# Performance work log

Hardware: AMD Instinct MI355X
Metric: run time of the kernel (lower is better)

## Reference

```python
import jax, jax.numpy as jnp
import numpy as np

DIM = 768
HEADS = 12
HEAD_DIM = DIM // HEADS
EPS_ATTN = 1e-6
LN_EPS = 1e-5


def _piece_weight():
    # BlockDistanceConv with num_patches_per_side=16, patch_group_size=16 -> 4x4 blocks
    bps = 4
    centers = np.array([[i + 0.5, j + 0.5] for i in range(bps) for j in range(bps)], dtype=np.float32)
    d = np.linalg.norm(centers[:, None, :] - centers[None, :, :], axis=-1)
    mat = np.cos(d / d.max() * np.pi / 4.0)  # 'cos' transform
    mat = mat / mat.sum(axis=0, keepdims=True)
    return jnp.asarray(mat, dtype=jnp.float32)  # [16, 16], out = W @ x over piece channels


def setup_inputs() -> dict:
    key = jax.random.key(0)
    ks = jax.random.split(key, 4)
    B, N, W, C = 128, 16, 16, DIM
    x = jax.random.normal(ks[0], (B, N, W, C), dtype=jnp.float32)
    ln_gamma = jnp.ones((C,), dtype=jnp.float32)
    ln_beta = jnp.zeros((C,), dtype=jnp.float32)
    w_qkv = jax.random.normal(ks[1], (C, 3 * C), dtype=jnp.float32) * (C ** -0.5)
    w_out = jax.random.normal(ks[2], (C, C), dtype=jnp.float32) * (C ** -0.5)
    b_out = jnp.zeros((C,), dtype=jnp.float32)
    w_piece = _piece_weight()
    return {"x": x, "ln_gamma": ln_gamma, "ln_beta": ln_beta, "w_qkv": w_qkv,
            "w_out": w_out, "b_out": b_out, "w_piece": w_piece}


def reference(x, ln_gamma, ln_beta, w_qkv, w_out, b_out, w_piece):
    B, N, W, C = x.shape
    H, D = HEADS, HEAD_DIM
    # LayerNorm over channel dim
    mu = jnp.mean(x, axis=-1, keepdims=True)
    var = jnp.mean((x - mu) ** 2, axis=-1, keepdims=True)
    xn = (x - mu) * jax.lax.rsqrt(var + LN_EPS) * ln_gamma + ln_beta
    # qkv projection (no bias)
    qkv = xn @ w_qkv  # [B,N,W,3C]
    q, k, v = jnp.split(qkv, 3, axis=-1)
    # relu kernel feature map
    q = jax.nn.relu(q) + EPS_ATTN
    k = jax.nn.relu(k) + EPS_ATTN
    # split heads: 'b n w (h d) -> b h n w d'
    def heads(t):
        return t.reshape(B, N, W, H, D).transpose(0, 3, 1, 2, 4)
    q, k, v = heads(q), heads(k), heads(v)
    # per-window kv = k^T v  (sum over window positions w)  -> [B,H,N,D,D]
    kv = jnp.einsum('bhnwd,bhnwe->bhnde', k, v)
    # BlockDistanceConv: 1x1 conv mixing over piece dim N with fixed weights
    kv = jnp.einsum('ij,bhjde->bhide', w_piece, kv)
    # out = q @ kv  -> [B,H,N,W,D]
    out = jnp.einsum('bhnwd,bhnde->bhnwe', q, kv)
    # merge heads: 'b h n w d -> b n w (h d)'
    out = out.transpose(0, 2, 3, 1, 4).reshape(B, N, W, H * D)
    # output projection (dropout is identity in eval)
    return out @ w_out + b_out
```

## Files before the change

kernel.cpp:

```cpp
#include <hip/hip_runtime.h>

#define DIM 768
#define HEADS 12
#define TOK 32768

typedef unsigned short ushort_t;
typedef __attribute__((ext_vector_type(8))) short short8v;
typedef __attribute__((ext_vector_type(4))) float f32x4;
typedef __attribute__((ext_vector_type(4))) unsigned short us4;

__device__ __forceinline__ ushort_t f2bf(float x) {
  union { float f; unsigned u; } c; c.f = x;
  unsigned r = (c.u + 0x7FFFu + ((c.u >> 16) & 1u)) >> 16;
  return (ushort_t)r;
}

__device__ __forceinline__ void gload_lds16(const void* g, void* l) {
  __builtin_amdgcn_global_load_lds((const __attribute__((address_space(1))) void*)g,
                                   (__attribute__((address_space(3))) void*)l, 16, 0, 0);
}

#define FENCE asm volatile("" ::: "memory")
#define SCHED0 __builtin_amdgcn_sched_barrier(0)
#define BARRIER do { FENCE; SCHED0; __builtin_amdgcn_s_barrier(); SCHED0; FENCE; } while (0)
#define LGK0 asm volatile("s_waitcnt lgkmcnt(0)" ::: "memory")
#define VM0  asm volatile("s_waitcnt vmcnt(0)" ::: "memory")
#define VM3  asm volatile("s_waitcnt vmcnt(3)" ::: "memory")

__global__ __launch_bounds__(256) void ln_kernel(const float* __restrict__ x,
                                                 const float* __restrict__ g,
                                                 const float* __restrict__ be,
                                                 ushort_t* __restrict__ xn) {
  int lane = threadIdx.x & 63;
  int row = blockIdx.x * 4 + (threadIdx.x >> 6);
  const float4* rx = (const float4*)(x + (size_t)row * DIM);
  float4 v[3];
  float s = 0.f, sq = 0.f;
  #pragma unroll
  for (int c = 0; c < 3; ++c) {
    v[c] = rx[lane + 64 * c];
    s  += v[c].x + v[c].y + v[c].z + v[c].w;
    sq += v[c].x * v[c].x + v[c].y * v[c].y + v[c].z * v[c].z + v[c].w * v[c].w;
  }
  #pragma unroll
  for (int off = 32; off; off >>= 1) {
    s  += __shfl_xor(s, off);
    sq += __shfl_xor(sq, off);
  }
  float mu  = s * (1.0f / DIM);
  float var = sq * (1.0f / DIM) - mu * mu;
  float rs  = rsqrtf(var + 1e-5f);
  us4* orow = (us4*)(xn + (size_t)row * DIM);
  const float4* gv = (const float4*)g;
  const float4* bv = (const float4*)be;
  #pragma unroll
  for (int c = 0; c < 3; ++c) {
    float4 gg = gv[lane + 64 * c];
    float4 bb = bv[lane + 64 * c];
    us4 pk;
    pk[0] = f2bf((v[c].x - mu) * rs * gg.x + bb.x);
    pk[1] = f2bf((v[c].y - mu) * rs * gg.y + bb.y);
    pk[2] = f2bf((v[c].z - mu) * rs * gg.z + bb.z);
    pk[3] = f2bf((v[c].w - mu) * rs * gg.w + bb.w);
    orow[lane + 64 * c] = pk;
  }
}

__global__ __launch_bounds__(256) void convT2(const float* __restrict__ s0,
                                              ushort_t* __restrict__ d0,
                                              const float* __restrict__ s1,
                                              ushort_t* __restrict__ d1) {
  int z = blockIdx.z;
  if (z && blockIdx.x >= DIM / 32) return;
  const float* src = z ? s1 : s0;
  ushort_t* dst = z ? d1 : d0;
  int Ccol = z ? DIM : 3 * DIM;
  const int R = DIM;
  __shared__ float tile[32][33];
  int c0 = blockIdx.x * 32, r0 = blockIdx.y * 32;
  int tx = threadIdx.x & 31, ty = threadIdx.x >> 5;
  #pragma unroll
  for (int i = 0; i < 32; i += 8)
    tile[ty + i][tx] = src[(size_t)(r0 + ty + i) * Ccol + c0 + tx];
  __syncthreads();
  #pragma unroll
  for (int i = 0; i < 32; i += 8)
    dst[(size_t)(c0 + ty + i) * R + r0 + tx] = f2bf(tile[tx][ty + i]);
}

__global__ __launch_bounds__(512, 2) void gemm_8ph(const ushort_t* __restrict__ A,
                                                   const ushort_t* __restrict__ Bt,
                                                   ushort_t* __restrict__ qbf,
                                                   ushort_t* __restrict__ kbf,
                                                   ushort_t* __restrict__ vTbf) {
  extern __shared__ __align__(16) char lds[];
  const int Kb = DIM * 2;
  const int N = 3 * DIM;
  const int nbn = N / 256;
  const size_t GHalf = (size_t)64 * Kb;

  int bid = blockIdx.x;
  int qd = gridDim.x >> 3;
  int wid = (bid & 7) * qd + (bid >> 3);
  int bm = wid / nbn, bn = wid % nbn;
  int row0 = bm * 256, col0 = bn * 256;
  int t = threadIdx.x;
  int lane = t & 63, wave = t >> 6;
  int wr = wave >> 2, wc = wave & 3;

  const char* Ag = (const char*)A + (size_t)row0 * Kb;
  const char* Bg = (const char*)Bt + (size_t)col0 * Kb;

  int o0 = t * 16;
  int sr = o0 >> 7;
  int skb = (o0 & 127) ^ ((sr & 7) << 4);
  size_t goff = (size_t)sr * Kb + skb;

  #define STG(Gbase, Lbase, kt)                                               \
    do {                                                                      \
      gload_lds16((Gbase) + goff + (size_t)(kt) * 128, lds + (Lbase) + o0);   \
      gload_lds16((Gbase) + goff + GHalf + (size_t)(kt) * 128,                \
                  lds + (Lbase) + o0 + 8192);                                 \
    } while (0)

  int fr = lane & 15, fkb = (lane >> 4) << 4;
  int swz = (fr & 7) << 4;
  int kb0 = fkb ^ swz;
  int kb1 = (64 + fkb) ^ swz;
  int laA = (wr * 128 + fr) * 128;
  int laB = 32768 + (wc * 64 + fr) * 128;

  #define LOAD_A(dst, dbase, mq)                                              \
    _Pragma("unroll") for (int mi = 0; mi < 4; ++mi) {                        \
      dst[mi][0] = *(const short8v*)(lds + (dbase) + laA + (mq)*8192 + mi*2048 + kb0); \
      dst[mi][1] = *(const short8v*)(lds + (dbase) + laA + (mq)*8192 + mi*2048 + kb1); \
    }
  #define LOAD_B(dst, dbase, nq)                                              \
    _Pragma("unroll") for (int ni = 0; ni < 2; ++ni) {                        \
      dst[ni][0] = *(const short8v*)(lds + (dbase) + laB + (nq)*4096 + ni*2048 + kb0); \
      dst[ni][1] = *(const short8v*)(lds + (dbase) + laB + (nq)*4096 + ni*2048 + kb1); \
    }
  #define MFMA16(av, bv, mq, nq)                                              \
    do {                                                                      \
      SCHED0;                                                                 \
      __builtin_amdgcn_s_setprio(1);                                          \
      _Pragma("unroll") for (int mi = 0; mi < 4; ++mi)                        \
        _Pragma("unroll") for (int ni = 0; ni < 2; ++ni) {                    \
          acc[(mq)*4+mi][(nq)*2+ni] = __builtin_amdgcn_mfma_f32_16x16x32_bf16(\
              av[mi][0], bv[ni][0], acc[(mq)*4+mi][(nq)*2+ni], 0, 0, 0);      \
          acc[(mq)*4+mi][(nq)*2+ni] = __builtin_amdgcn_mfma_f32_16x16x32_bf16(\
              av[mi][1], bv[ni][1], acc[(mq)*4+mi][(nq)*2+ni], 0, 0, 0);      \
        }                                                                     \
      __builtin_amdgcn_s_setprio(0);                                          \
    } while (0)

  STG(Ag, 0, 0);  STG(Ag + 128 * Kb, 16384, 0);
  STG(Bg, 32768, 0);  STG(Bg + 128 * Kb, 49152, 0);
  STG(Ag, 65536, 1);  STG(Ag + 128 * Kb, 65536 + 16384, 1);
  STG(Bg, 65536 + 32768, 1);
  asm volatile("s_waitcnt vmcnt(6)" ::: "memory");
  BARRIER;

  short8v aR0[4][2], aR1[4][2], bR0[2][2], bR1[2][2];
  LOAD_A(aR0, 0, 0); LOAD_B(bR0, 0, 0);

  f32x4 acc[8][4] = {};
  for (int it = 0; it < 6; ++it) {
    const int d0 = 0, d1 = 65536;
    int t1k = 2 * it + 1, t2k = 2 * it + 2, t3k = 2 * it + 3;
    bool st = (it < 5);
    LOAD_A(aR1, d0, 1);
    STG(Bg + 128 * Kb, d1 + 49152, t1k);
    MFMA16(aR0, bR0, 0, 0);
    BARRIER;
    LOAD_B(bR1, d0, 1);
    MFMA16(aR1, bR0, 1, 0);
    BARRIER;
    if (st) { STG(Ag, d0, t2k); STG(Ag + 128 * Kb, d0 + 16384, t2k); }
    MFMA16(aR0, bR1, 0, 1);
    if (st) asm volatile("s_waitcnt vmcnt(4)" ::: "memory");
    else    asm volatile("s_waitcnt vmcnt(0)" ::: "memory");
    BARRIER;
    LOAD_A(aR0, d1, 0); LOAD_B(bR0, d1, 0);
    if (st) STG(Bg, d0 + 32768, t2k);
    MFMA16(aR1, bR1, 1, 1);
    BARRIER;
    LOAD_A(aR1, d1, 1);
    if (st) STG(Bg + 128 * Kb, d0 + 49152, t2k);
    MFMA16(aR0, bR0, 0, 0);
    BARRIER;
    LOAD_B(bR1, d1, 1);
    MFMA16(aR1, bR0, 1, 0);
    BARRIER;
    if (st) { STG(Ag, d1, t3k); STG(Ag + 128 * Kb, d1 + 16384, t3k); }
    MFMA16(aR0, bR1, 0, 1);
    if (st) asm volatile("s_waitcnt vmcnt(4)" ::: "memory");
    BARRIER;
    if (st) {
      LOAD_A(aR0, d0, 0); LOAD_B(bR0, d0, 0);
      STG(Bg, d1 + 32768, t3k);
    }
    MFMA16(aR1, bR1, 1, 1);
    BARRIER;
  }
  #undef STG
  #undef LOAD_A
  #undef LOAD_B
  #undef MFMA16

  int rbase = row0 + wr * 128 + ((lane >> 4) << 2);
  int cbase = col0 + wc * 64 + fr;
  #pragma unroll
  for (int m = 0; m < 8; ++m) {
    int r0r = rbase + m * 16;
    #pragma unroll
    for (int n = 0; n < 4; ++n) {
      int c = cbase + n * 16;
      if (c < DIM) {
        #pragma unroll
        for (int j = 0; j < 4; ++j)
          qbf[(size_t)(r0r + j) * DIM + c] = f2bf(fmaxf(acc[m][n][j], 0.0f) + 1e-6f);
      } else if (c < 2 * DIM) {
        #pragma unroll
        for (int j = 0; j < 4; ++j)
          kbf[(size_t)(r0r + j) * DIM + (c - DIM)] = f2bf(fmaxf(acc[m][n][j], 0.0f) + 1e-6f);
      } else {
        int ch = c - 2 * DIM;
        int hh = ch >> 6, e = ch & 63;
        int bb = r0r >> 8, rr = r0r & 255;
        us4 pk;
        #pragma unroll
        for (int j = 0; j < 4; ++j) pk[j] = f2bf(acc[m][n][j]);
        *(us4*)&vTbf[((((size_t)bb * HEADS + hh) * 64 + e) << 8) + rr] = pk;
      }
    }
  }
}

__global__ __launch_bounds__(512, 4) void gemm_out8(const ushort_t* __restrict__ A,
                                                    const ushort_t* __restrict__ Bt,
                                                    const float* __restrict__ bias,
                                                    float* __restrict__ C) {
  extern __shared__ __align__(16) char lds[];
  const int Kb = DIM * 2;
  const int N = DIM;
  const int nbn = N / 128;
  const int NT = DIM / 32;

  int bid = blockIdx.x;
  int qd = gridDim.x >> 3;
  int wid = (bid & 7) * qd + (bid >> 3);
  int bm = wid / nbn, bn = wid % nbn;
  int row0 = bm * 256, col0 = bn * 128;
  int t = threadIdx.x;
  int lane = t & 63, wave = t >> 6;
  int wr = wave >> 1, wc = wave & 1;

  const char* Ag = (const char*)A + (size_t)row0 * Kb;
  const char* Bg = (const char*)Bt + (size_t)col0 * Kb;

  int oA0 = t * 16, oA1 = 8192 + t * 16;
  int rA0 = oA0 >> 6, rA1 = oA1 >> 6;
  size_t gA0 = (size_t)rA0 * Kb + ((oA0 & 63) ^ ((rA0 & 3) << 4));
  size_t gA1 = (size_t)rA1 * Kb + ((oA1 & 63) ^ ((rA1 & 3) << 4));
  int oB = t * 16;
  int rB = oB >> 6;
  size_t gB = (size_t)rB * Kb + ((oB & 63) ^ ((rB & 3) << 4));

  #define STG2(tile, slot)                                                    \
    do {                                                                      \
      char* sb = lds + (slot) * 24576;                                        \
      size_t kk = (size_t)(tile) * 64;                                        \
      gload_lds16(Ag + gA0 + kk, sb + oA0);                                   \
      gload_lds16(Ag + gA1 + kk, sb + oA1);                                   \
      gload_lds16(Bg + gB + kk, sb + 16384 + oB);                             \
    } while (0)

  int fr = lane & 15, fkb = (lane >> 4) << 4;
  int kb = fkb ^ ((fr & 3) << 4);
  int aoff = (wr * 64 + fr) * 64 + kb;
  int boff = 16384 + (wc * 64 + fr) * 64 + kb;

  STG2(0, 0);

  f32x4 acc[4][4] = {};
  for (int kt = 0; kt < NT; ++kt) {
    int cur = kt & 1;
    if (kt + 1 < NT) { STG2(kt + 1, cur ^ 1); VM3; }
    else VM0;
    BARRIER;
    const char* sb = lds + cur * 24576;
    short8v a[4], b[4];
    #pragma unroll
    for (int mi = 0; mi < 4; ++mi) a[mi] = *(const short8v*)(sb + aoff + mi * 1024);
    #pragma unroll
    for (int ni = 0; ni < 4; ++ni) b[ni] = *(const short8v*)(sb + boff + ni * 1024);
    SCHED0;
    __builtin_amdgcn_s_setprio(1);
    #pragma unroll
    for (int mi = 0; mi < 4; ++mi)
      #pragma unroll
      for (int ni = 0; ni < 4; ++ni)
        acc[mi][ni] = __builtin_amdgcn_mfma_f32_16x16x32_bf16(a[mi], b[ni], acc[mi][ni], 0, 0, 0);
    __builtin_amdgcn_s_setprio(0);
    BARRIER;
  }
  #undef STG2

  int rbase = row0 + wr * 64 + ((lane >> 4) << 2);
  int cbase = col0 + wc * 64 + fr;
  #pragma unroll
  for (int m = 0; m < 4; ++m) {
    #pragma unroll
    for (int n = 0; n < 4; ++n) {
      int c = cbase + n * 16;
      float bz = bias[c];
      #pragma unroll
      for (int j = 0; j < 4; ++j)
        C[(size_t)(rbase + m * 16 + j) * N + c] = acc[m][n][j] + bz;
    }
  }
}

__global__ __launch_bounds__(512, 4) void attn_fused(const ushort_t* __restrict__ qbf,
                                                     const ushort_t* __restrict__ kbf,
                                                     const ushort_t* __restrict__ vTbf,
                                                     const float* __restrict__ wp,
                                                     ushort_t* __restrict__ attnO) {
  extern __shared__ __align__(16) char lds[];
  const int QOFF = 32768, SOFF = 40960;
  int bh = blockIdx.x;
  int b = bh / HEADS, h = bh % HEADS;
  int t = threadIdx.x;
  int lane = t & 63, wave = t >> 6;
  int fr = lane & 15, fkb = (lane >> 4) << 4;
  int lg4 = (lane >> 4) << 2;

  const char* qg = (const char*)(qbf + ((size_t)b * 256) * DIM + h * 64);
  const char* kg = (const char*)(kbf + ((size_t)b * 256) * DIM + h * 64);
  const char* vg = (const char*)(vTbf + ((size_t)bh << 14));

  #pragma unroll
  for (int is = 0; is < 4; ++is) {
    int o = is * 8192 + t * 16;
    int r = o >> 7;
    int byt = (o & 127) ^ ((r & 7) << 4);
    gload_lds16(kg + (size_t)r * (DIM * 2) + byt, lds + o);
  }
  {
    int o = t * 16;
    int r = o >> 7;
    int byt = (o & 127) ^ ((r & 7) << 4);
    gload_lds16(qg + (size_t)r * (DIM * 2) + byt, lds + QOFF + o);
  }
  #pragma unroll
  for (int is = 0; is < 4; ++is) {
    int o = is * 8192 + t * 16;
    int e = o >> 9;
    int byt = (o & 511) ^ ((e & 7) << 4);
    gload_lds16(vg + e * 512 + byt, lds + SOFF + o);
  }
  VM0;
  __builtin_amdgcn_s_barrier();

  int wrs = wave & 3, wcs = wave >> 2;
  int wrp = wave >> 2, wcp = wave & 3;

  short8v vt[8];
  {
    int e = wcp * 16 + fr;
    int es = (e & 7) << 4;
    #pragma unroll
    for (int ks = 0; ks < 8; ++ks)
      vt[ks] = *(const short8v*)(lds + SOFF + e * 512 + ((ks * 64 + fkb) ^ es));
  }
  LGK0;
  BARRIER;

  for (int q4 = 0; q4 < 4; ++q4) {
    f32x4 accA[4][2] = {};
    {
      short8v qf[2][2];
      #pragma unroll
      for (int ni = 0; ni < 2; ++ni) {
        int r = wcs * 32 + ni * 16 + fr;
        int rs = (r & 7) << 4;
        qf[ni][0] = *(const short8v*)(lds + QOFF + r * 128 + (fkb ^ rs));
        qf[ni][1] = *(const short8v*)(lds + QOFF + r * 128 + ((64 + fkb) ^ rs));
      }
      #pragma unroll
      for (int mi = 0; mi < 4; ++mi) {
        int r = wrs * 64 + mi * 16 + fr;
        int rs = (r & 7) << 4;
        short8v kf0 = *(const short8v*)(lds + r * 128 + (fkb ^ rs));
        short8v kf1 = *(const short8v*)(lds + r * 128 + ((64 + fkb) ^ rs));
        #pragma unroll
        for (int ni = 0; ni < 2; ++ni) {
          accA[mi][ni] = __builtin_amdgcn_mfma_f32_16x16x32_bf16(kf0, qf[ni][0], accA[mi][ni], 0, 0, 0);
          accA[mi][ni] = __builtin_amdgcn_mfma_f32_16x16x32_bf16(kf1, qf[ni][1], accA[mi][ni], 0, 0, 0);
        }
      }
    }
    BARRIER;
    #pragma unroll
    for (int mi = 0; mi < 4; ++mi)
      #pragma unroll
      for (int ni = 0; ni < 2; ++ni) {
        float wpf = wp[(q4 * 4 + wcs * 2 + ni) * 16 + wrs * 4 + mi];
        us4 pk;
        #pragma unroll
        for (int j = 0; j < 4; ++j) pk[j] = f2bf(accA[mi][ni][j] * wpf);
        int qrow = wcs * 32 + ni * 16 + fr;
        int sbyte = (wrs * 64 + mi * 16 + lg4) * 2;
        *(us4*)(lds + SOFF + qrow * 512 + (sbyte ^ ((qrow & 7) << 4))) = pk;
      }
    if (q4 < 3) {
      int o = t * 16;
      int r = o >> 7;
      int byt = (o & 127) ^ ((r & 7) << 4);
      gload_lds16(qg + (size_t)((q4 + 1) * 64 + r) * (DIM * 2) + byt, lds + QOFF + o);
    }
    LGK0;
    BARRIER;
    f32x4 accB[2] = {{0.f,0.f,0.f,0.f},{0.f,0.f,0.f,0.f}};
    #pragma unroll
    for (int ks = 0; ks < 8; ++ks) {
      int kbq = ks * 64 + fkb;
      #pragma unroll
      for (int mt = 0; mt < 2; ++mt) {
        int r = wrp * 32 + mt * 16 + fr;
        short8v av = *(const short8v*)(lds + SOFF + r * 512 + (kbq ^ ((r & 7) << 4)));
        accB[mt] = __builtin_amdgcn_mfma_f32_16x16x32_bf16(av, vt[ks], accB[mt], 0, 0, 0);
      }
    }
    #pragma unroll
    for (int mt = 0; mt < 2; ++mt) {
      int row = b * 256 + q4 * 64 + wrp * 32 + mt * 16 + lg4;
      int col = h * 64 + wcp * 16 + fr;
      #pragma unroll
      for (int j = 0; j < 4; ++j)
        attnO[(size_t)(row + j) * DIM + col] = f2bf(accB[mt][j]);
    }
    if (q4 < 3) asm volatile("s_waitcnt vmcnt(8)" ::: "memory");
    BARRIER;
  }
}

extern "C" void kernel_launch(void* const* d_in, const int* in_sizes, int n_in,
                              void* d_out, int out_size, void* d_ws, size_t ws_size,
                              hipStream_t stream) {
  const float* x    = (const float*)d_in[0];
  const float* g    = (const float*)d_in[1];
  const float* be   = (const float*)d_in[2];
  const float* wqkv = (const float*)d_in[3];
  const float* wout = (const float*)d_in[4];
  const float* bout = (const float*)d_in[5];
  const float* wp   = (const float*)d_in[6];
  float* out = (float*)d_out;

  char* w = (char*)d_ws;
  const size_t SZ = (size_t)TOK * DIM * 2;
  ushort_t* qbf   = (ushort_t*)(w);
  ushort_t* kbf   = (ushort_t*)(w + SZ);
  ushort_t* vTbf  = (ushort_t*)(w + 2 * SZ);
  ushort_t* xn    = (ushort_t*)(w + 3 * SZ);
  ushort_t* wqkvT = (ushort_t*)(w + 4 * SZ);
  ushort_t* woutT = (ushort_t*)(w + 4 * SZ + 3538944);
  ushort_t* attnO = xn;

  (void)hipFuncSetAttribute(reinterpret_cast<const void*>(&gemm_8ph),
                            hipFuncAttributeMaxDynamicSharedMemorySize, 131072);
  (void)hipFuncSetAttribute(reinterpret_cast<const void*>(&gemm_out8),
                            hipFuncAttributeMaxDynamicSharedMemorySize, 49152);
  (void)hipFuncSetAttribute(reinterpret_cast<const void*>(&attn_fused),
                            hipFuncAttributeMaxDynamicSharedMemorySize, 73728);

  dim3 gct(3 * DIM / 32, DIM / 32, 2);
  convT2<<<gct, 256, 0, stream>>>(wqkv, wqkvT, wout, woutT);

  ln_kernel<<<TOK / 4, 256, 0, stream>>>(x, g, be, xn);

  gemm_8ph<<<(TOK / 256) * (3 * DIM / 256), 512, 131072, stream>>>(
      xn, wqkvT, qbf, kbf, vTbf);

  attn_fused<<<128 * HEADS, 512, 73728, stream>>>(qbf, kbf, vTbf, wp, attnO);

  gemm_out8<<<(TOK / 256) * (DIM / 128), 512, 49152, stream>>>(
      attnO, woutT, bout, out);
}
```

Measured before the change: 269.1 us.

## Replace 8-phase 256x256 QKV GEMM with simpler 256x128 double-buffered kernel

The QKV projection GEMM drops its hand-scheduled 8-phase 256x256 tile kernel with 128KB of LDS. It now uses the same 256x128 tile, 32-wide K step, double-buffered structure as the output GEMM, with 48KB of LDS and launch bounds allowing 4 blocks per CU. This trades per-block data reuse and the fine-grained interleaving of loads and MFMAs for higher occupancy and twice as many blocks. It also doubles the number of K iterations and barriers.

New measurement: 273.1 us. Within noise of the previous version (+1.5%).

```diff
diff --git a/kernel.cpp b/kernel.cpp
--- a/kernel.cpp
+++ b/kernel.cpp
@@ -88,7 +88,7 @@
     dst[(size_t)(c0 + ty + i) * R + r0 + tx] = f2bf(tile[tx][ty + i]);
 }
 
-__global__ __launch_bounds__(512, 2) void gemm_8ph(const ushort_t* __restrict__ A,
+__global__ __launch_bounds__(512, 4) void gemm_qkv(const ushort_t* __restrict__ A,
                                                    const ushort_t* __restrict__ Bt,
                                                    ushort_t* __restrict__ qbf,
                                                    ushort_t* __restrict__ kbf,
@@ -96,122 +96,73 @@
   extern __shared__ __align__(16) char lds[];
   const int Kb = DIM * 2;
   const int N = 3 * DIM;
-  const int nbn = N / 256;
-  const size_t GHalf = (size_t)64 * Kb;
+  const int nbn = N / 128;
+  const int NT = DIM / 32;
 
   int bid = blockIdx.x;
   int qd = gridDim.x >> 3;
   int wid = (bid & 7) * qd + (bid >> 3);
   int bm = wid / nbn, bn = wid % nbn;
-  int row0 = bm * 256, col0 = bn * 256;
+  int row0 = bm * 256, col0 = bn * 128;
   int t = threadIdx.x;
   int lane = t & 63, wave = t >> 6;
-  int wr = wave >> 2, wc = wave & 3;
+  int wr = wave >> 1, wc = wave & 1;
 
   const char* Ag = (const char*)A + (size_t)row0 * Kb;
   const char* Bg = (const char*)Bt + (size_t)col0 * Kb;
 
-  int o0 = t * 16;
-  int sr = o0 >> 7;
-  int skb = (o0 & 127) ^ ((sr & 7) << 4);
-  size_t goff = (size_t)sr * Kb + skb;
-
-  #define STG(Gbase, Lbase, kt)                                               \
+  int oA0 = t * 16, oA1 = 8192 + t * 16;
+  int rA0 = oA0 >> 6, rA1 = oA1 >> 6;
+  size_t gA0 = (size_t)rA0 * Kb + ((oA0 & 63) ^ ((rA0 & 3) << 4));
+  size_t gA1 = (size_t)rA1 * Kb + ((oA1 & 63) ^ ((rA1 & 3) << 4));
+  int oB = t * 16;
+  int rB = oB >> 6;
+  size_t gB = (size_t)rB * Kb + ((oB & 63) ^ ((rB & 3) << 4));
+
+  #define STG1(tile_, slot)                                                   \
     do {                                                                      \
-      gload_lds16((Gbase) + goff + (size_t)(kt) * 128, lds + (Lbase) + o0);   \
-      gload_lds16((Gbase) + goff + GHalf + (size_t)(kt) * 128,                \
-                  lds + (Lbase) + o0 + 8192);                                 \
+      char* sb = lds + (slot) * 24576;                                        \
+      size_t kk = (size_t)(tile_) * 64;                                       \
+      gload_lds16(Ag + gA0 + kk, sb + oA0);                                   \
+      gload_lds16(Ag + gA1 + kk, sb + oA1);                                   \
+      gload_lds16(Bg + gB + kk, sb + 16384 + oB);                             \
     } while (0)
 
   int fr = lane & 15, fkb = (lane >> 4) << 4;
-  int swz = (fr & 7) << 4;
-  int kb0 = fkb ^ swz;
-  int kb1 = (64 + fkb) ^ swz;
-  int laA = (wr * 128 + fr) * 128;
-  int laB = 32768 + (wc * 64 + fr) * 128;
-
-  #define LOAD_A(dst, dbase, mq)                                              \
-    _Pragma("unroll") for (int mi = 0; mi < 4; ++mi) {                        \
-      dst[mi][0] = *(const short8v*)(lds + (dbase) + laA + (mq)*8192 + mi*2048 + kb0); \
-      dst[mi][1] = *(const short8v*)(lds + (dbase) + laA + (mq)*8192 + mi*2048 + kb1); \
-    }
-  #define LOAD_B(dst, dbase, nq)                                              \
-    _Pragma("unroll") for (int ni = 0; ni < 2; ++ni) {                        \
-      dst[ni][0] = *(const short8v*)(lds + (dbase) + laB + (nq)*4096 + ni*2048 + kb0); \
-      dst[ni][1] = *(const short8v*)(lds + (dbase) + laB + (nq)*4096 + ni*2048 + kb1); \
-    }
-  #define MFMA16(av, bv, mq, nq)                                              \
-    do {                                                                      \
-      SCHED0;                                                                 \
-      __builtin_amdgcn_s_setprio(1);                                          \
-      _Pragma("unroll") for (int mi = 0; mi < 4; ++mi)                        \
-        _Pragma("unroll") for (int ni = 0; ni < 2; ++ni) {                    \
-          acc[(mq)*4+mi][(nq)*2+ni] = __builtin_amdgcn_mfma_f32_16x16x32_bf16(\
-              av[mi][0], bv[ni][0], acc[(mq)*4+mi][(nq)*2+ni], 0, 0, 0);      \
-          acc[(mq)*4+mi][(nq)*2+ni] = __builtin_amdgcn_mfma_f32_16x16x32_bf16(\
-              av[mi][1], bv[ni][1], acc[(mq)*4+mi][(nq)*2+ni], 0, 0, 0);      \
-        }                                                                     \
-      __builtin_amdgcn_s_setprio(0);                                          \
-    } while (0)
-
-  STG(Ag, 0, 0);  STG(Ag + 128 * Kb, 16384, 0);
-  STG(Bg, 32768, 0);  STG(Bg + 128 * Kb, 49152, 0);
-  STG(Ag, 65536, 1);  STG(Ag + 128 * Kb, 65536 + 16384, 1);
-  STG(Bg, 65536 + 32768, 1);
-  asm volatile("s_waitcnt vmcnt(6)" ::: "memory");
-  BARRIER;
-
-  short8v aR0[4][2], aR1[4][2], bR0[2][2], bR1[2][2];
-  LOAD_A(aR0, 0, 0); LOAD_B(bR0, 0, 0);
-
-  f32x4 acc[8][4] = {};
-  for (int it = 0; it < 6; ++it) {
-    const int d0 = 0, d1 = 65536;
-    int t1k = 2 * it + 1, t2k = 2 * it + 2, t3k = 2 * it + 3;
-    bool st = (it < 5);
-    LOAD_A(aR1, d0, 1);
-    STG(Bg + 128 * Kb, d1 + 49152, t1k);
-    MFMA16(aR0, bR0, 0, 0);
-    BARRIER;
-    LOAD_B(bR1, d0, 1);
-    MFMA16(aR1, bR0, 1, 0);
-    BARRIER;
-    if (st) { STG(Ag, d0, t2k); STG(Ag + 128 * Kb, d0 + 16384, t2k); }
-    MFMA16(aR0, bR1, 0, 1);
-    if (st) asm volatile("s_waitcnt vmcnt(4)" ::: "memory");
-    else    asm volatile("s_waitcnt vmcnt(0)" ::: "memory");
-    BARRIER;
-    LOAD_A(aR0, d1, 0); LOAD_B(bR0, d1, 0);
-    if (st) STG(Bg, d0 + 32768, t2k);
-    MFMA16(aR1, bR1, 1, 1);
-    BARRIER;
-    LOAD_A(aR1, d1, 1);
-    if (st) STG(Bg + 128 * Kb, d0 + 49152, t2k);
-    MFMA16(aR0, bR0, 0, 0);
-    BARRIER;
-    LOAD_B(bR1, d1, 1);
-    MFMA16(aR1, bR0, 1, 0);
-    BARRIER;
-    if (st) { STG(Ag, d1, t3k); STG(Ag + 128 * Kb, d1 + 16384, t3k); }
-    MFMA16(aR0, bR1, 0, 1);
-    if (st) asm volatile("s_waitcnt vmcnt(4)" ::: "memory");
-    BARRIER;
-    if (st) {
-      LOAD_A(aR0, d0, 0); LOAD_B(bR0, d0, 0);
-      STG(Bg, d1 + 32768, t3k);
-    }
-    MFMA16(aR1, bR1, 1, 1);
-    BARRIER;
-  }
-  #undef STG
-  #undef LOAD_A
-  #undef LOAD_B
-  #undef MFMA16
-
-  int rbase = row0 + wr * 128 + ((lane >> 4) << 2);
+  int kb = fkb ^ ((fr & 3) << 4);
+  int aoff = (wr * 64 + fr) * 64 + kb;
+  int boff = 16384 + (wc * 64 + fr) * 64 + kb;
+
+  STG1(0, 0);
+
+  f32x4 acc[4][4] = {};
+  for (int kt = 0; kt < NT; ++kt) {
+    int cur = kt & 1;
+    if (kt + 1 < NT) { STG1(kt + 1, cur ^ 1); VM3; }
+    else VM0;
+    BARRIER;
+    const char* sb = lds + cur * 24576;
+    short8v a[4], b[4];
+    #pragma unroll
+    for (int mi = 0; mi < 4; ++mi) a[mi] = *(const short8v*)(sb + aoff + mi * 1024);
+    #pragma unroll
+    for (int ni = 0; ni < 4; ++ni) b[ni] = *(const short8v*)(sb + boff + ni * 1024);
+    SCHED0;
+    __builtin_amdgcn_s_setprio(1);
+    #pragma unroll
+    for (int mi = 0; mi < 4; ++mi)
+      #pragma unroll
+      for (int ni = 0; ni < 4; ++ni)
+        acc[mi][ni] = __builtin_amdgcn_mfma_f32_16x16x32_bf16(a[mi], b[ni], acc[mi][ni], 0, 0, 0);
+    __builtin_amdgcn_s_setprio(0);
+    BARRIER;
+  }
+  #undef STG1
+
+  int rbase = row0 + wr * 64 + ((lane >> 4) << 2);
   int cbase = col0 + wc * 64 + fr;
   #pragma unroll
-  for (int m = 0; m < 8; ++m) {
+  for (int m = 0; m < 4; ++m) {
     int r0r = rbase + m * 16;
     #pragma unroll
     for (int n = 0; n < 4; ++n) {
@@ -267,10 +218,10 @@
   int rB = oB >> 6;
   size_t gB = (size_t)rB * Kb + ((oB & 63) ^ ((rB & 3) << 4));
 
-  #define STG2(tile, slot)                                                    \
+  #define STG2(tile_, slot)                                                   \
     do {                                                                      \
       char* sb = lds + (slot) * 24576;                                        \
-      size_t kk = (size_t)(tile) * 64;                                        \
+      size_t kk = (size_t)(tile_) * 64;                                       \
       gload_lds16(Ag + gA0 + kk, sb + oA0);                                   \
       gload_lds16(Ag + gA1 + kk, sb + oA1);                                   \
       gload_lds16(Bg + gB + kk, sb + 16384 + oB);                             \
@@ -468,8 +419,8 @@
   ushort_t* woutT = (ushort_t*)(w + 4 * SZ + 3538944);
   ushort_t* attnO = xn;
 
-  (void)hipFuncSetAttribute(reinterpret_cast<const void*>(&gemm_8ph),
-                            hipFuncAttributeMaxDynamicSharedMemorySize, 131072);
+  (void)hipFuncSetAttribute(reinterpret_cast<const void*>(&gemm_qkv),
+                            hipFuncAttributeMaxDynamicSharedMemorySize, 49152);
   (void)hipFuncSetAttribute(reinterpret_cast<const void*>(&gemm_out8),
                             hipFuncAttributeMaxDynamicSharedMemorySize, 49152);
   (void)hipFuncSetAttribute(reinterpret_cast<const void*>(&attn_fused),
@@ -480,7 +431,7 @@
 
   ln_kernel<<<TOK / 4, 256, 0, stream>>>(x, g, be, xn);
 
-  gemm_8ph<<<(TOK / 256) * (3 * DIM / 256), 512, 131072, stream>>>(
+  gemm_qkv<<<(TOK / 256) * (3 * DIM / 128), 512, 49152, stream>>>(
       xn, wqkvT, qbf, kbf, vTbf);
 
   attn_fused<<<128 * HEADS, 512, 73728, stream>>>(qbf, kbf, vTbf, wp, attnO);
```
